# Optimization experiments

Hardware: AMD Instinct MI355X
Metric: run time of the kernel (lower is better)

## Reference

```python
import jax, jax.numpy as jnp
import numpy as np

N_NODES = 20000
N_EDGES = 256000
F_IN = 1024
HID = 1000
N_CLS = 1000
NEG_SLOPE = 0.2


def _glorot(key, shape):
    fan_in, fan_out = shape[1], shape[0]
    lim = np.sqrt(6.0 / (fan_in + fan_out))
    return jax.random.uniform(key, shape, jnp.float32, -lim, lim)


def setup_inputs() -> dict:
    key = jax.random.key(0)
    ks = jax.random.split(key, 16)
    x = jax.random.normal(ks[0], (N_NODES, F_IN), jnp.float32)
    edge_index = jax.random.randint(ks[1], (2, N_EDGES), 0, N_NODES, jnp.int64)
    edge_attr = jax.random.uniform(ks[2], (N_EDGES, 1), jnp.float32)
    return {
        "x": x,
        "edge_index": edge_index,
        "edge_attr": edge_attr,
        # conv1 params (GATv2Conv: F_IN -> HID, heads=1, edge_dim=1)
        "w1_l": _glorot(ks[3], (HID, F_IN)),
        "b1_l": jnp.zeros((HID,), jnp.float32),
        "w1_r": _glorot(ks[4], (HID, F_IN)),
        "b1_r": jnp.zeros((HID,), jnp.float32),
        "w1_e": _glorot(ks[5], (HID, 1)),
        "att1": _glorot(ks[6], (1, HID))[0],
        "bias1": jnp.zeros((HID,), jnp.float32),
        # conv2 params (HID -> N_CLS, heads=1, concat=False)
        "w2_l": _glorot(ks[7], (N_CLS, HID)),
        "b2_l": jnp.zeros((N_CLS,), jnp.float32),
        "w2_r": _glorot(ks[8], (N_CLS, HID)),
        "b2_r": jnp.zeros((N_CLS,), jnp.float32),
        "w2_e": _glorot(ks[9], (N_CLS, 1)),
        "att2": _glorot(ks[10], (1, N_CLS))[0],
        "bias2": jnp.zeros((N_CLS,), jnp.float32),
    }


def gatv2_layer(x, src, dst, edge_attr, Wl, bl, Wr, br, We, att, bias):
    # GATv2Conv with heads=1 (eval mode: attention dropout inactive).
    n = x.shape[0]
    xl = x @ Wl.T + bl                       # source-side transform [N, C]
    xr = x @ Wr.T + br                       # target-side transform [N, C]
    e = xl[src] + xr[dst] + edge_attr @ We.T  # per-edge features [E, C]
    e = jax.nn.leaky_relu(e, NEG_SLOPE)
    logits = e @ att                          # [E]
    # segment softmax over incoming edges of each target node
    m = jax.ops.segment_max(logits, dst, num_segments=n)
    alpha = jnp.exp(logits - m[dst])
    denom = jax.ops.segment_sum(alpha, dst, num_segments=n)
    alpha = alpha / (denom[dst] + 1e-16)
    out = jax.ops.segment_sum(xl[src] * alpha[:, None], dst, num_segments=n)
    return out + bias


def reference(x, edge_index, edge_attr,
              w1_l, b1_l, w1_r, b1_r, w1_e, att1, bias1,
              w2_l, b2_l, w2_r, b2_r, w2_e, att2, bias2):
    src, dst = edge_index[0], edge_index[1]
    # feature dropout (p=0.6) is identity in eval mode
    h = gatv2_layer(x, src, dst, edge_attr, w1_l, b1_l, w1_r, b1_r, w1_e, att1, bias1)
    h = jax.nn.relu(h)
    h = gatv2_layer(h, src, dst, edge_attr, w2_l, b2_l, w2_r, b2_r, w2_e, att2, bias2)
    return jax.nn.sigmoid(h)
```

## Files before the change

### kernel.cpp

```cpp
#include <hip/hip_runtime.h>
#include <math.h>

#define N_NODES 20000
#define N_EDGES 256000
#define F_IN 1024
#define C_DIM 1000
#define NEG_SLOPE 0.2f

#define MPAD 20096
#define KDIM 1024
#define NW 2048

typedef __attribute__((ext_vector_type(8))) short          bf16x8;
typedef __attribute__((ext_vector_type(8))) unsigned short u16x8;
typedef __attribute__((ext_vector_type(4))) float          f32x4;
typedef unsigned short us;

__device__ __forceinline__ us f2bf(float f) {
  unsigned u = __float_as_uint(f);
  return (us)((u + 0x7FFFu + ((u >> 16) & 1u)) >> 16);
}
__device__ __forceinline__ float bf2f(us u) {
  return __uint_as_float(((unsigned)u) << 16);
}

__device__ __forceinline__ void gld16(void* lds, const void* g) {
  __builtin_amdgcn_global_load_lds(
      (const __attribute__((address_space(1))) unsigned int*)g,
      (__attribute__((address_space(3))) unsigned int*)lds, 16, 0, 0);
}

__global__ void count_k(const int* __restrict__ edst, int* __restrict__ counts) {
  int e = blockIdx.x * blockDim.x + threadIdx.x;
  if (e < N_EDGES) atomicAdd(&counts[edst[e]], 1);
}

__global__ __launch_bounds__(1024)
void scan_k(const int* __restrict__ counts, int* __restrict__ row_ptr, int* __restrict__ cursor) {
  __shared__ int sm[1024];
  int t = threadIdx.x;
  int base = t * 20;
  int loc[20];
  int run = 0;
#pragma unroll
  for (int i = 0; i < 20; ++i) {
    int idx = base + i;
    int v = (idx < N_NODES) ? counts[idx] : 0;
    run += v;
    loc[i] = run;
  }
  sm[t] = run;
  __syncthreads();
  for (int off = 1; off < 1024; off <<= 1) {
    int v = (t >= off) ? sm[t - off] : 0;
    __syncthreads();
    sm[t] += v;
    __syncthreads();
  }
  int excl = (t > 0) ? sm[t - 1] : 0;
#pragma unroll
  for (int i = 0; i < 20; ++i) {
    int idx = base + i;
    if (idx < N_NODES) {
      int e = excl + ((i > 0) ? loc[i - 1] : 0);
      row_ptr[idx] = e;
      cursor[idx] = e;
    }
  }
  if (t == 0) row_ptr[N_NODES] = sm[1023];
}

__global__ void scatter_k(const int* __restrict__ esrc, const float* __restrict__ eattr,
                          const int* __restrict__ edst, int* __restrict__ cursor,
                          int2* __restrict__ spair) {
  int e = blockIdx.x * blockDim.x + threadIdx.x;
  if (e < N_EDGES) {
    int p = atomicAdd(&cursor[edst[e]], 1);
    spair[p] = make_int2(esrc[e], __float_as_int(eattr[e]));
  }
}

__global__ void cvt_pad_k(const float* __restrict__ src, us* __restrict__ dst,
                          int R, int C, int dstRows) {
  long total = (long)dstRows * 256;
  for (long i = (long)blockIdx.x * blockDim.x + threadIdx.x; i < total;
       i += (long)gridDim.x * blockDim.x) {
    int row = (int)(i >> 8);
    int c = ((int)(i & 255)) << 2;
    ushort4 o = make_ushort4(0, 0, 0, 0);
    if (row < R && c < C) {
      float4 v = *(const float4*)(src + (long)row * C + c);
      o.x = f2bf(v.x); o.y = f2bf(v.y); o.z = f2bf(v.z); o.w = f2bf(v.w);
    }
    *(ushort4*)(dst + ((long)row << 10) + c) = o;
  }
}

__global__ __launch_bounds__(256)
void gemm_mfma_k(const us* __restrict__ Abf, const us* __restrict__ Wbf,
                 const float* __restrict__ bl, const float* __restrict__ br,
                 us* __restrict__ Cbf) {
  __shared__ us As0[4096], As1[4096], Bs0[4096], Bs1[4096];
  const int tid = threadIdx.x;
  const int lane = tid & 63;
  const int wv = tid >> 6;
  const int wr = wv >> 1, wc = wv & 1;

  const int nwg = gridDim.x;
  const int q = nwg >> 3;
  const int wg = (blockIdx.x & 7) * q + (blockIdx.x >> 3);
  const long bm = (long)(wg >> 4) * 128;
  const long bn = (long)(wg & 15) * 128;

  f32x4 acc[4][4];
  const f32x4 z4 = {0.f, 0.f, 0.f, 0.f};
#pragma unroll
  for (int i = 0; i < 4; ++i)
#pragma unroll
    for (int j = 0; j < 4; ++j) acc[i][j] = z4;

  const int i0 = tid, i1 = tid + 256;
  const us* gA0 = Abf + (bm + (i0 >> 2)) * KDIM + (i0 & 3) * 8;
  const us* gA1 = Abf + (bm + (i1 >> 2)) * KDIM + (i1 & 3) * 8;
  const us* gB0 = Wbf + (bn + (i0 >> 2)) * KDIM + (i0 & 3) * 8;
  const us* gB1 = Wbf + (bn + (i1 >> 2)) * KDIM + (i1 & 3) * 8;

  const int g = lane >> 4;
  const int rA = lane & 15;

  gld16(As0 + wv * 512, gA0);
  gld16(As0 + 2048 + wv * 512, gA1);
  gld16(Bs0 + wv * 512, gB0);
  gld16(Bs0 + 2048 + wv * 512, gB1);
  __syncthreads();

  for (int t = 0; t < 32; ++t) {
    if (t + 1 < 32) {
      int kn = (t + 1) << 5;
      us* dA = ((t + 1) & 1) ? As1 : As0;
      us* dB = ((t + 1) & 1) ? Bs1 : Bs0;
      gld16(dA + wv * 512, gA0 + kn);
      gld16(dA + 2048 + wv * 512, gA1 + kn);
      gld16(dB + wv * 512, gB0 + kn);
      gld16(dB + 2048 + wv * 512, gB1 + kn);
    }
    const us* Ar = (t & 1) ? As1 : As0;
    const us* Br = (t & 1) ? Bs1 : Bs0;
    bf16x8 av[4], bv[4];
#pragma unroll
    for (int mi = 0; mi < 4; ++mi)
      av[mi] = *(const bf16x8*)&Ar[(wr * 64 + mi * 16 + rA) * 32 + g * 8];
#pragma unroll
    for (int ni = 0; ni < 4; ++ni)
      bv[ni] = *(const bf16x8*)&Br[(wc * 64 + ni * 16 + rA) * 32 + g * 8];
#pragma unroll
    for (int mi = 0; mi < 4; ++mi)
#pragma unroll
      for (int ni = 0; ni < 4; ++ni)
        acc[mi][ni] = __builtin_amdgcn_mfma_f32_16x16x32_bf16(av[mi], bv[ni], acc[mi][ni], 0, 0, 0);
    __syncthreads();
  }

  int coln[4]; float biasv[4]; int cok[4];
#pragma unroll
  for (int ni = 0; ni < 4; ++ni) {
    coln[ni] = (int)bn + wc * 64 + ni * 16 + rA;
    int cm = coln[ni] & 1023;
    cok[ni] = (cm < C_DIM);
    biasv[ni] = cok[ni] ? ((coln[ni] < 1024) ? bl[cm] : br[cm]) : 0.f;
  }
#pragma unroll
  for (int mi = 0; mi < 4; ++mi) {
#pragma unroll
    for (int j = 0; j < 4; ++j) {
      int row = (int)bm + wr * 64 + mi * 16 + g * 4 + j;
      if (row < N_NODES) {
#pragma unroll
        for (int ni = 0; ni < 4; ++ni)
          if (cok[ni])
            Cbf[(long)row * NW + coln[ni]] = f2bf(acc[mi][ni][j] + biasv[ni]);
      }
    }
  }
}

template <int ACT>
__global__ __launch_bounds__(256)
void edge_agg_k(const us* __restrict__ xlr, const int2* __restrict__ spair,
                const int* __restrict__ row_ptr,
                const float* __restrict__ We, const float* __restrict__ att,
                const float* __restrict__ bias, us* __restrict__ hout,
                float* __restrict__ fout) {
  const int wave = threadIdx.x >> 6;
  const int lane = threadIdx.x & 63;
  const int q0 = lane, q1 = lane + 64;
  const bool ok1 = (q1 < 125);

  const int d = (blockIdx.x << 2) | wave;
  if (d >= N_NODES) return;

  float attv[2][8], wev[2][8];
#pragma unroll
  for (int j = 0; j < 2; ++j) {
    int qq = lane + 64 * j;
    if (qq < 125) {
      float4 a0 = ((const float4*)att)[2 * qq], a1 = ((const float4*)att)[2 * qq + 1];
      float4 w0 = ((const float4*)We)[2 * qq],  w1 = ((const float4*)We)[2 * qq + 1];
      attv[j][0] = a0.x; attv[j][1] = a0.y; attv[j][2] = a0.z; attv[j][3] = a0.w;
      attv[j][4] = a1.x; attv[j][5] = a1.y; attv[j][6] = a1.z; attv[j][7] = a1.w;
      wev[j][0] = w0.x; wev[j][1] = w0.y; wev[j][2] = w0.z; wev[j][3] = w0.w;
      wev[j][4] = w1.x; wev[j][5] = w1.y; wev[j][6] = w1.z; wev[j][7] = w1.w;
    } else {
#pragma unroll
      for (int t = 0; t < 8; ++t) { attv[j][t] = 0.f; wev[j][t] = 0.f; }
    }
  }

  const int beg = row_ptr[d];
  const int end = row_ptr[d + 1];

  float xrv[2][8];
  {
    const u16x8* xrp = (const u16x8*)(xlr + (long)d * NW + 1024);
#pragma unroll
    for (int j = 0; j < 2; ++j) {
      int qq = lane + 64 * j;
      if (qq < 125) {
        u16x8 h = xrp[qq];
#pragma unroll
        for (int t = 0; t < 8; ++t) xrv[j][t] = bf2f(h[t]);
      } else {
#pragma unroll
        for (int t = 0; t < 8; ++t) xrv[j][t] = 0.f;
      }
    }
  }

  float m = -INFINITY, denom = 0.f;
  float acc[2][8];
#pragma unroll
  for (int j = 0; j < 2; ++j)
#pragma unroll
    for (int t = 0; t < 8; ++t) acc[j][t] = 0.f;

#define EDGE_LOGIT(PAIR, VH0, VH1, PART)                                   \
  {                                                                        \
    const u16x8* xs = (const u16x8*)(xlr + (long)(PAIR).x * NW);           \
    float ea = __int_as_float((PAIR).y);                                   \
    VH0 = xs[q0];                                                          \
    if (ok1) VH1 = xs[q1];                                                 \
    else { u16x8 zz = {0,0,0,0,0,0,0,0}; VH1 = zz; }                       \
    PART = 0.f;                                                            \
    _Pragma("unroll")                                                      \
    for (int t = 0; t < 8; ++t) {                                          \
      float tt = bf2f(VH0[t]) + xrv[0][t] + ea * wev[0][t];                \
      tt = (tt >= 0.f) ? tt : NEG_SLOPE * tt;                              \
      PART = fmaf(attv[0][t], tt, PART);                                   \
      float uu = bf2f(VH1[t]) + xrv[1][t] + ea * wev[1][t];                \
      uu = (uu >= 0.f) ? uu : NEG_SLOPE * uu;                              \
      PART = fmaf(attv[1][t], uu, PART);                                   \
    }                                                                      \
  }

#define ONLINE_UPDATE(PART, VH0, VH1)                                      \
  {                                                                        \
    if ((PART) > m) {                                                      \
      float sc = __expf(m - (PART));                                       \
      denom = denom * sc + 1.f;                                            \
      _Pragma("unroll")                                                    \
      for (int t = 0; t < 8; ++t) {                                        \
        acc[0][t] = fmaf(acc[0][t], sc, bf2f(VH0[t]));                     \
        acc[1][t] = fmaf(acc[1][t], sc, bf2f(VH1[t]));                     \
      }                                                                    \
      m = (PART);                                                          \
    } else {                                                               \
      float w = __expf((PART) - m);                                        \
      denom += w;                                                          \
      _Pragma("unroll")                                                    \
      for (int t = 0; t < 8; ++t) {                                        \
        acc[0][t] = fmaf(w, bf2f(VH0[t]), acc[0][t]);                      \
        acc[1][t] = fmaf(w, bf2f(VH1[t]), acc[1][t]);                      \
      }                                                                    \
    }                                                                      \
  }

  int i = beg;
  for (; i + 2 <= end; i += 2) {
    int2 p0 = spair[i], p1 = spair[i + 1];
    u16x8 a0, a1, b0, b1;
    float pt0, pt1;
    EDGE_LOGIT(p0, a0, a1, pt0);
    EDGE_LOGIT(p1, b0, b1, pt1);
#pragma unroll
    for (int off = 32; off > 0; off >>= 1) {
      pt0 += __shfl_xor(pt0, off, 64);
      pt1 += __shfl_xor(pt1, off, 64);
    }
    ONLINE_UPDATE(pt0, a0, a1);
    ONLINE_UPDATE(pt1, b0, b1);
  }
  if (i < end) {
    int2 p0 = spair[i];
    u16x8 a0, a1;
    float pt0;
    EDGE_LOGIT(p0, a0, a1, pt0);
#pragma unroll
    for (int off = 32; off > 0; off >>= 1) pt0 += __shfl_xor(pt0, off, 64);
    ONLINE_UPDATE(pt0, a0, a1);
  }
#undef EDGE_LOGIT
#undef ONLINE_UPDATE

  float inv = 1.f / (denom + 1e-16f);
  if (ACT == 0) {
    us* orow = hout + ((long)d << 10);
#pragma unroll
    for (int j = 0; j < 2; ++j) {
      int qq = lane + 64 * j;
      u16x8 pk = {0, 0, 0, 0, 0, 0, 0, 0};
      if (qq < 125) {
        const float4 b0 = ((const float4*)bias)[2 * qq], b1 = ((const float4*)bias)[2 * qq + 1];
        const float bb[8] = {b0.x, b0.y, b0.z, b0.w, b1.x, b1.y, b1.z, b1.w};
#pragma unroll
        for (int t = 0; t < 8; ++t)
          pk[t] = f2bf(fmaxf(fmaf(acc[j][t], inv, bb[t]), 0.f));
      }
      ((u16x8*)orow)[qq] = pk;
    }
  } else {
#pragma unroll
    for (int j = 0; j < 2; ++j) {
      int qq = lane + 64 * j;
      if (qq < 125) {
        const float4 b0 = ((const float4*)bias)[2 * qq], b1 = ((const float4*)bias)[2 * qq + 1];
        const float bb[8] = {b0.x, b0.y, b0.z, b0.w, b1.x, b1.y, b1.z, b1.w};
        float o[8];
#pragma unroll
        for (int t = 0; t < 8; ++t)
          o[t] = 1.f / (1.f + __expf(-fmaf(acc[j][t], inv, bb[t])));
        float4* op = (float4*)(fout + (long)d * C_DIM + 8 * qq);
        op[0] = make_float4(o[0], o[1], o[2], o[3]);
        op[1] = make_float4(o[4], o[5], o[6], o[7]);
      }
    }
  }
}

extern "C" void kernel_launch(void* const* d_in, const int* in_sizes, int n_in,
                              void* d_out, int out_size, void* d_ws, size_t ws_size,
                              hipStream_t stream) {
  const float* x     = (const float*)d_in[0];
  const int*   ei    = (const int*)d_in[1];
  const float* eattr = (const float*)d_in[2];
  const float* w1l   = (const float*)d_in[3];
  const float* b1l   = (const float*)d_in[4];
  const float* w1r   = (const float*)d_in[5];
  const float* b1r   = (const float*)d_in[6];
  const float* w1e   = (const float*)d_in[7];
  const float* att1  = (const float*)d_in[8];
  const float* bias1 = (const float*)d_in[9];
  const float* w2l   = (const float*)d_in[10];
  const float* b2l   = (const float*)d_in[11];
  const float* w2r   = (const float*)d_in[12];
  const float* b2r   = (const float*)d_in[13];
  const float* w2e   = (const float*)d_in[14];
  const float* att2  = (const float*)d_in[15];
  const float* bias2 = (const float*)d_in[16];
  float* out = (float*)d_out;

  char* w = (char*)d_ws;
  us*  xlr  = (us*)w;
  us*  Abf  = (us*)(w + 82313216L);
  us*  W21  = (us*)(w + 123469824L);
  us*  W22  = (us*)(w + 127664128L);
  int2* spair = (int2*)(w + 131858432L);
  int* row_ptr = (int*)(w + 133906432L);
  int* cursor  = row_ptr + (N_NODES + 1);
  int* counts  = cursor + N_NODES;

  const int* esrc = ei;
  const int* edst = ei + N_EDGES;

  hipMemsetAsync(counts, 0, N_NODES * sizeof(int), stream);
  count_k<<<(N_EDGES + 255) / 256, 256, 0, stream>>>(edst, counts);
  scan_k<<<1, 1024, 0, stream>>>(counts, row_ptr, cursor);
  scatter_k<<<(N_EDGES + 255) / 256, 256, 0, stream>>>(esrc, eattr, edst, cursor, spair);

  cvt_pad_k<<<1024, 256, 0, stream>>>(w1l, W21, C_DIM, F_IN, 1024);
  cvt_pad_k<<<1024, 256, 0, stream>>>(w1r, W21 + 1024 * 1024, C_DIM, F_IN, 1024);
  cvt_pad_k<<<1024, 256, 0, stream>>>(w2l, W22, C_DIM, C_DIM, 1024);
  cvt_pad_k<<<1024, 256, 0, stream>>>(w2r, W22 + 1024 * 1024, C_DIM, C_DIM, 1024);

  cvt_pad_k<<<4096, 256, 0, stream>>>(x, Abf, N_NODES, F_IN, MPAD);
  gemm_mfma_k<<<2512, 256, 0, stream>>>(Abf, W21, b1l, b1r, xlr);
  edge_agg_k<0><<<N_NODES / 4, 256, 0, stream>>>(xlr, spair, row_ptr, w1e, att1, bias1,
                                                 Abf, nullptr);

  gemm_mfma_k<<<2512, 256, 0, stream>>>(Abf, W22, b2l, b2r, xlr);
  edge_agg_k<1><<<N_NODES / 4, 256, 0, stream>>>(xlr, spair, row_ptr, w2e, att2, bias2,
                                                 nullptr, out);
}
```

Before: 524.9 us.

## Fuse conversion kernels, swizzle GEMM LDS layout, use nontemporal output stores

Merges the five fp32-to-bf16 conversion launches into a single block-partitioned kernel, which cuts launch overhead and lets the small conversions overlap with the large one. Applies an XOR swizzle to the 16-byte chunk placement in the GEMM's shared-memory tiles so the MFMA operand reads hit fewer LDS bank conflicts. Writes the aggregation outputs with nontemporal stores to reduce cache pollution. The swizzle must match between the global-to-LDS load and the LDS read, and nontemporal stores of the bf16 hidden layer could hurt if that data is reread soon from cache by the second GEMM.

Measured after the change: 524.3 us. About the same (-0.1%).

```diff
diff --git a/kernel.cpp b/kernel.cpp
--- a/kernel.cpp
+++ b/kernel.cpp
@@ -80,11 +80,11 @@
   }
 }
 
-__global__ void cvt_pad_k(const float* __restrict__ src, us* __restrict__ dst,
-                          int R, int C, int dstRows) {
+__device__ __forceinline__ void cvt_body(const float* __restrict__ src, us* __restrict__ dst,
+                                         int R, int C, int dstRows, int nblk, int bid,
+                                         int tid) {
   long total = (long)dstRows * 256;
-  for (long i = (long)blockIdx.x * blockDim.x + threadIdx.x; i < total;
-       i += (long)gridDim.x * blockDim.x) {
+  for (long i = (long)bid * 256 + tid; i < total; i += (long)nblk * 256) {
     int row = (int)(i >> 8);
     int c = ((int)(i & 255)) << 2;
     ushort4 o = make_ushort4(0, 0, 0, 0);
@@ -94,6 +94,19 @@
     }
     *(ushort4*)(dst + ((long)row << 10) + c) = o;
   }
+}
+
+__global__ __launch_bounds__(256)
+void cvt_all_k(const float* __restrict__ x,
+               const float* __restrict__ w1l, const float* __restrict__ w1r,
+               const float* __restrict__ w2l, const float* __restrict__ w2r,
+               us* __restrict__ Abf, us* __restrict__ W21, us* __restrict__ W22) {
+  int b = blockIdx.x, tid = threadIdx.x;
+  if (b < 4096)      cvt_body(x,   Abf,            N_NODES, F_IN,  MPAD, 4096, b,        tid);
+  else if (b < 5120) cvt_body(w1l, W21,            C_DIM,   F_IN,  1024, 1024, b - 4096, tid);
+  else if (b < 6144) cvt_body(w1r, W21 + 1048576,  C_DIM,   F_IN,  1024, 1024, b - 5120, tid);
+  else if (b < 7168) cvt_body(w2l, W22,            C_DIM,   C_DIM, 1024, 1024, b - 6144, tid);
+  else               cvt_body(w2r, W22 + 1048576,  C_DIM,   C_DIM, 1024, 1024, b - 7168, tid);
 }
 
 __global__ __launch_bounds__(256)
@@ -120,13 +133,16 @@
     for (int j = 0; j < 4; ++j) acc[i][j] = z4;
 
   const int i0 = tid, i1 = tid + 256;
-  const us* gA0 = Abf + (bm + (i0 >> 2)) * KDIM + (i0 & 3) * 8;
-  const us* gA1 = Abf + (bm + (i1 >> 2)) * KDIM + (i1 & 3) * 8;
-  const us* gB0 = Wbf + (bn + (i0 >> 2)) * KDIM + (i0 & 3) * 8;
-  const us* gB1 = Wbf + (bn + (i1 >> 2)) * KDIM + (i1 & 3) * 8;
+  const int c0 = (i0 & 3) ^ ((i0 >> 2) & 3);
+  const int c1 = (i1 & 3) ^ ((i1 >> 2) & 3);
+  const us* gA0 = Abf + (bm + (i0 >> 2)) * KDIM + c0 * 8;
+  const us* gA1 = Abf + (bm + (i1 >> 2)) * KDIM + c1 * 8;
+  const us* gB0 = Wbf + (bn + (i0 >> 2)) * KDIM + c0 * 8;
+  const us* gB1 = Wbf + (bn + (i1 >> 2)) * KDIM + c1 * 8;
 
   const int g = lane >> 4;
   const int rA = lane & 15;
+  const int kbs = (g ^ (rA & 3)) << 3;
 
   gld16(As0 + wv * 512, gA0);
   gld16(As0 + 2048 + wv * 512, gA1);
@@ -149,10 +165,10 @@
     bf16x8 av[4], bv[4];
 #pragma unroll
     for (int mi = 0; mi < 4; ++mi)
-      av[mi] = *(const bf16x8*)&Ar[(wr * 64 + mi * 16 + rA) * 32 + g * 8];
+      av[mi] = *(const bf16x8*)&Ar[(wr * 64 + mi * 16 + rA) * 32 + kbs];
 #pragma unroll
     for (int ni = 0; ni < 4; ++ni)
-      bv[ni] = *(const bf16x8*)&Br[(wc * 64 + ni * 16 + rA) * 32 + g * 8];
+      bv[ni] = *(const bf16x8*)&Br[(wc * 64 + ni * 16 + rA) * 32 + kbs];
 #pragma unroll
     for (int mi = 0; mi < 4; ++mi)
 #pragma unroll
@@ -325,7 +341,7 @@
         for (int t = 0; t < 8; ++t)
           pk[t] = f2bf(fmaxf(fmaf(acc[j][t], inv, bb[t]), 0.f));
       }
-      ((u16x8*)orow)[qq] = pk;
+      __builtin_nontemporal_store(pk, &((u16x8*)orow)[qq]);
     }
   } else {
 #pragma unroll
@@ -338,9 +354,11 @@
 #pragma unroll
         for (int t = 0; t < 8; ++t)
           o[t] = 1.f / (1.f + __expf(-fmaf(acc[j][t], inv, bb[t])));
-        float4* op = (float4*)(fout + (long)d * C_DIM + 8 * qq);
-        op[0] = make_float4(o[0], o[1], o[2], o[3]);
-        op[1] = make_float4(o[4], o[5], o[6], o[7]);
+        f32x4* op = (f32x4*)(fout + (long)d * C_DIM + 8 * qq);
+        f32x4 v0 = {o[0], o[1], o[2], o[3]};
+        f32x4 v1 = {o[4], o[5], o[6], o[7]};
+        __builtin_nontemporal_store(v0, op);
+        __builtin_nontemporal_store(v1, op + 1);
       }
     }
   }
@@ -381,17 +399,13 @@
   const int* esrc = ei;
   const int* edst = ei + N_EDGES;
 
-  hipMemsetAsync(counts, 0, N_NODES * sizeof(int), stream);
+  (void)hipMemsetAsync(counts, 0, N_NODES * sizeof(int), stream);
   count_k<<<(N_EDGES + 255) / 256, 256, 0, stream>>>(edst, counts);
   scan_k<<<1, 1024, 0, stream>>>(counts, row_ptr, cursor);
   scatter_k<<<(N_EDGES + 255) / 256, 256, 0, stream>>>(esrc, eattr, edst, cursor, spair);
 
-  cvt_pad_k<<<1024, 256, 0, stream>>>(w1l, W21, C_DIM, F_IN, 1024);
-  cvt_pad_k<<<1024, 256, 0, stream>>>(w1r, W21 + 1024 * 1024, C_DIM, F_IN, 1024);
-  cvt_pad_k<<<1024, 256, 0, stream>>>(w2l, W22, C_DIM, C_DIM, 1024);
-  cvt_pad_k<<<1024, 256, 0, stream>>>(w2r, W22 + 1024 * 1024, C_DIM, C_DIM, 1024);
-
-  cvt_pad_k<<<4096, 256, 0, stream>>>(x, Abf, N_NODES, F_IN, MPAD);
+  cvt_all_k<<<8192, 256, 0, stream>>>(x, w1l, w1r, w2l, w2r, Abf, W21, W22);
+
   gemm_mfma_k<<<2512, 256, 0, stream>>>(Abf, W21, b1l, b1r, xlr);
   edge_agg_k<0><<<N_NODES / 4, 256, 0, stream>>>(xlr, spair, row_ptr, w1e, att1, bias1,
                                                  Abf, nullptr);
```
